# Optimization experiments

Measured on AMD Instinct MI355X. Metric: run time of the kernel, lower is better.

Reference implementation:

```python
import jax, jax.numpy as jnp
import numpy as np

N_NODES = 100000
N_PAIRS = 800000  # undirected pairs; E = 2*N_PAIRS directed edges
D_FEAT = 128
THRESHOLD = 0.01
EPS = 1e-8


def setup_inputs() -> dict:
    key = jax.random.key(0)
    k1, k2, k3, k4 = jax.random.split(key, 4)
    # symmetric edge list without self-loops (each undirected pair in both directions)
    src = jax.random.randint(k1, (N_PAIRS,), 0, N_NODES)
    off = jax.random.randint(k2, (N_PAIRS,), 1, N_NODES)
    dst = (src + off) % N_NODES  # guaranteed != src
    edge_index = jnp.stack([jnp.concatenate([src, dst]),
                            jnp.concatenate([dst, src])]).astype(jnp.int64)
    w_half = jax.random.uniform(k3, (N_PAIRS,), dtype=jnp.float32)
    edge_weight = jnp.concatenate([w_half, w_half])
    features = jax.random.normal(k4, (N_NODES, D_FEAT), dtype=jnp.float32)
    return {"edge_index": edge_index, "edge_weight": edge_weight, "features": features}


def reference(edge_index, edge_weight, features):
    # Cosine-similarity edge dropping (Jaccard.forward, non-binary feature path).
    # Original: build NxN sparse adj, take triu, per-edge cosine sim, zero edges
    # with sim < threshold, symmetrize (triu + triu^T), read back at edge positions.
    # For a symmetric duplicate-free edge list this equals per-edge masking, with
    # diagonal entries doubled by triu + triu^T.
    src, dst = edge_index[0], edge_index[1]
    node_norm = jnp.sqrt(jnp.sum(features * features, axis=-1))  # [N]
    inner = jnp.sum(features[src] * features[dst], axis=-1)       # [E] per-edge gather+dot
    sim = inner / (node_norm[src] * node_norm[dst] + EPS)
    keep = (sim >= THRESHOLD).astype(edge_weight.dtype)
    diag_double = 1.0 + (src == dst).astype(edge_weight.dtype)    # triu+triu^T doubles diagonal
    return edge_weight * keep * diag_double
```

## Files before the change

kernel.cpp:

```cpp
#include <hip/hip_runtime.h>
#include <hip/hip_fp16.h>

#define D_FEAT 128
#define THRESH 0.01f
#define EPS_F  1e-8f


__device__ float edge_out_scalar(const float* __restrict__ feat,
                                 float w, int s, int d) {
#pragma clang fp contract(off)
    const float* fs = feat + (size_t)s * D_FEAT;
    const float* fd = feat + (size_t)d * D_FEAT;
    float r[8], rs[8], rd[8];
#pragma unroll
    for (int j = 0; j < 8; ++j) {
        float a = fs[j], b = fd[j];
        r[j]  = a * b;
        rs[j] = a * a;
        rd[j] = b * b;
    }
    for (int k = 1; k < 16; ++k) {
#pragma unroll
        for (int j = 0; j < 8; ++j) {
            float a = fs[8 * k + j], b = fd[8 * k + j];
            r[j]  = r[j]  + a * b;
            rs[j] = rs[j] + a * a;
            rd[j] = rd[j] + b * b;
        }
    }
    float inner = ((r[0]  + r[1])  + (r[2]  + r[3]))  + ((r[4]  + r[5])  + (r[6]  + r[7]));
    float ss    = ((rs[0] + rs[1]) + (rs[2] + rs[3])) + ((rs[4] + rs[5]) + (rs[6] + rs[7]));
    float dd    = ((rd[0] + rd[1]) + (rd[2] + rd[3])) + ((rd[4] + rd[5]) + (rd[6] + rd[7]));
    float ns = __fsqrt_rn(ss);
    float nd = __fsqrt_rn(dd);
    float denom = ns * nd + EPS_F;
    float sim = inner / denom;
    float keep = (sim >= THRESH) ? 1.0f : 0.0f;
    float diag = (s == d) ? 2.0f : 1.0f;
    return (w * keep) * diag;
}

__device__ __forceinline__ float exact_sim_pairlanes(const float* __restrict__ feat,
                                                     int src, int dst, int h) {
#pragma clang fp contract(off)
    const float4* fs = (const float4*)(feat + (size_t)src * D_FEAT);
    const float4* fd = (const float4*)(feat + (size_t)dst * D_FEAT);
    float r[4], rs[4], rd[4];
    {
        float4 a = fs[h];
        float4 b = fd[h];
        r[0]  = a.x * b.x; r[1]  = a.y * b.y; r[2]  = a.z * b.z; r[3]  = a.w * b.w;
        rs[0] = a.x * a.x; rs[1] = a.y * a.y; rs[2] = a.z * a.z; rs[3] = a.w * a.w;
        rd[0] = b.x * b.x; rd[1] = b.y * b.y; rd[2] = b.z * b.z; rd[3] = b.w * b.w;
    }
#pragma unroll
    for (int k = 1; k < 16; ++k) {
        float4 a = fs[2 * k + h];
        float4 b = fd[2 * k + h];
        r[0]  = r[0]  + a.x * b.x;
        r[1]  = r[1]  + a.y * b.y;
        r[2]  = r[2]  + a.z * b.z;
        r[3]  = r[3]  + a.w * b.w;
        rs[0] = rs[0] + a.x * a.x;
        rs[1] = rs[1] + a.y * a.y;
        rs[2] = rs[2] + a.z * a.z;
        rs[3] = rs[3] + a.w * a.w;
        rd[0] = rd[0] + b.x * b.x;
        rd[1] = rd[1] + b.y * b.y;
        rd[2] = rd[2] + b.z * b.z;
        rd[3] = rd[3] + b.w * b.w;
    }
    float A  = (r[0]  + r[1])  + (r[2]  + r[3]);
    float As = (rs[0] + rs[1]) + (rs[2] + rs[3]);
    float Ad = (rd[0] + rd[1]) + (rd[2] + rd[3]);

    float inner = A  + __shfl_xor(A, 1, 64);
    float ssE   = As + __shfl_xor(As, 1, 64);
    float ddE   = Ad + __shfl_xor(Ad, 1, 64);

    float ns    = __fsqrt_rn(ssE);
    float nd    = __fsqrt_rn(ddE);
    float den   = ns * nd + EPS_F;
    return inner / den;
}

__global__ __launch_bounds__(256) void jaccard_edge_kernel(
    const int* __restrict__ ei, const float* __restrict__ w,
    const float* __restrict__ feat, float* __restrict__ out,
    int P, int E)
{
    int t    = blockIdx.x * blockDim.x + threadIdx.x;
    int pair = t >> 1;
    int half = t & 1;
    if (pair >= P) return;

    int src = ei[pair];
    int dst = ei[E + pair];

    float sim  = exact_sim_pairlanes(feat, src, dst, half);
    float keep = (sim >= THRESH) ? 1.0f : 0.0f;

    if (half == 0) {
        float diag = (src == dst) ? 2.0f : 1.0f;
        out[pair] = (w[pair] * keep) * diag;
        int m = P + pair;
        if (m < E) {
            int s2 = ei[m];
            int d2 = ei[E + m];
            if (s2 == dst && d2 == src) out[m] = (w[m] * keep) * diag;
            else                        out[m] = edge_out_scalar(feat, w[m], s2, d2);
        }
    }
}

__global__ __launch_bounds__(256) void convert_f16_kernel(
    const float* __restrict__ feat, __half* __restrict__ hfeat, int n8)
{
    int t = blockIdx.x * blockDim.x + threadIdx.x;
    if (t >= n8) return;
    const float4* p = (const float4*)feat + 2 * (size_t)t;
    float4 a = p[0];
    float4 b = p[1];
    __half2 h0 = __floats2half2_rn(a.x, a.y);
    __half2 h1 = __floats2half2_rn(a.z, a.w);
    __half2 h2 = __floats2half2_rn(b.x, b.y);
    __half2 h3 = __floats2half2_rn(b.z, b.w);
    uint4 o;
    o.x = *reinterpret_cast<unsigned int*>(&h0);
    o.y = *reinterpret_cast<unsigned int*>(&h1);
    o.z = *reinterpret_cast<unsigned int*>(&h2);
    o.w = *reinterpret_cast<unsigned int*>(&h3);
    reinterpret_cast<uint4*>(hfeat)[(size_t)t] = o;
}

__device__ __forceinline__ void acc2(unsigned int ua, unsigned int ub,
                                     float& dot, float& sab, float& ss, float& dd) {
    float2 fa = __half22float2(*reinterpret_cast<const __half2*>(&ua));
    float2 fb = __half22float2(*reinterpret_cast<const __half2*>(&ub));
    float p0 = fa.x * fb.x, p1 = fa.y * fb.y;
    dot += p0 + p1;
    sab += fabsf(p0) + fabsf(p1);
    ss  += fa.x * fa.x + fa.y * fa.y;
    dd  += fb.x * fb.x + fb.y * fb.y;
}

__global__ __launch_bounds__(256) void jaccard_edge_f16_kernel(
    const int* __restrict__ ei, const float* __restrict__ w,
    const float* __restrict__ feat, const __half* __restrict__ hfeat,
    float* __restrict__ out, int P, int E)
{
    int t    = blockIdx.x * blockDim.x + threadIdx.x;
    int pair = t >> 2;
    int q    = t & 3;
    if (pair >= P) return;

    int src = ei[pair];
    int dst = ei[E + pair];

    const uint4* ha = (const uint4*)(hfeat + (size_t)src * D_FEAT);
    const uint4* hb = (const uint4*)(hfeat + (size_t)dst * D_FEAT);

    float dot = 0.f, sab = 0.f, ss = 0.f, dd = 0.f;
#pragma unroll
    for (int k = 0; k < 4; ++k) {
        uint4 ua = ha[4 * k + q];
        uint4 ub = hb[4 * k + q];
        acc2(ua.x, ub.x, dot, sab, ss, dd);
        acc2(ua.y, ub.y, dot, sab, ss, dd);
        acc2(ua.z, ub.z, dot, sab, ss, dd);
        acc2(ua.w, ub.w, dot, sab, ss, dd);
    }
    dot += __shfl_xor(dot, 1, 64); dot += __shfl_xor(dot, 2, 64);
    sab += __shfl_xor(sab, 1, 64); sab += __shfl_xor(sab, 2, 64);
    ss  += __shfl_xor(ss,  1, 64); ss  += __shfl_xor(ss,  2, 64);
    dd  += __shfl_xor(dd,  1, 64); dd  += __shfl_xor(dd,  2, 64);

    float na  = __fsqrt_rn(ss);
    float nb  = __fsqrt_rn(dd);
    float den = na * nb + EPS_F;
    float sim = dot / den;

    float bnd = 1.2e-3f * (sab / den) + 1.2e-3f * fabsf(sim)
              + 3.5e-7f * (1.0f / na + 1.0f / nb) + 1e-7f;
    float diff = sim - THRESH;

    float keep;
    if (fabsf(diff) > bnd) {
        keep = (diff >= 0.f) ? 1.0f : 0.0f;
    } else {
        float se = 0.f;
        if (q < 2) se = exact_sim_pairlanes(feat, src, dst, q);
        keep = (se >= THRESH) ? 1.0f : 0.0f;
    }

    if (q == 0) {
        float diag = (src == dst) ? 2.0f : 1.0f;
        out[pair] = (w[pair] * keep) * diag;
        int m = P + pair;
        if (m < E) {
            int s2 = ei[m];
            int d2 = ei[E + m];
            if (s2 == dst && d2 == src) out[m] = (w[m] * keep) * diag;
            else                        out[m] = edge_out_scalar(feat, w[m], s2, d2);
        }
    }
}

extern "C" void kernel_launch(void* const* d_in, const int* in_sizes, int n_in,
                              void* d_out, int out_size, void* d_ws, size_t ws_size,
                              hipStream_t stream) {
    const int*   ei   = (const int*)d_in[0];
    const float* w    = (const float*)d_in[1];
    const float* feat = (const float*)d_in[2];
    float*       out  = (float*)d_out;

    int E = in_sizes[1];
    int P = E - E / 2;
    long nfeat = in_sizes[2];
    size_t need = (size_t)nfeat * sizeof(__half);

    if (ws_size < need || (nfeat & 7) != 0) {
        int threads = 2 * P;
        int grid = (threads + 255) / 256;
        jaccard_edge_kernel<<<grid, 256, 0, stream>>>(ei, w, feat, out, P, E);
        return;
    }

    __half* hfeat = (__half*)d_ws;
    int n8 = (int)(nfeat / 8);
    convert_f16_kernel<<<(n8 + 255) / 256, 256, 0, stream>>>(feat, hfeat, n8);

    int threads = 4 * P;
    int grid = (threads + 255) / 256;
    jaccard_edge_f16_kernel<<<grid, 256, 0, stream>>>(ei, w, feat, hfeat, out, P, E);
}
```

Before: 155.9 us.

## Precompute exact per-node norms and use fdot2 f16 dot with two lanes per pair

The conversion kernel now also computes each node's exact fp32 norm, using the same summation order as the original, and stores it in workspace. The edge kernel reads these norms, so it no longer reduces squared norms per edge, and it computes the half-precision dot product with packed fdot2 instructions, two lanes per pair. The fallback for borderline edges now only recomputes the exact inner product. Each lane holds more data in registers, and the error bound is a new heuristic that could misclassify edges if it is too loose.

```diff
diff --git a/kernel.cpp b/kernel.cpp
--- a/kernel.cpp
+++ b/kernel.cpp
@@ -4,6 +4,8 @@
 #define D_FEAT 128
 #define THRESH 0.01f
 #define EPS_F  1e-8f
+
+typedef _Float16 half2_t __attribute__((ext_vector_type(2)));
 
 
 __device__ float edge_out_scalar(const float* __restrict__ feat,
@@ -57,18 +59,12 @@
     for (int k = 1; k < 16; ++k) {
         float4 a = fs[2 * k + h];
         float4 b = fd[2 * k + h];
-        r[0]  = r[0]  + a.x * b.x;
-        r[1]  = r[1]  + a.y * b.y;
-        r[2]  = r[2]  + a.z * b.z;
-        r[3]  = r[3]  + a.w * b.w;
-        rs[0] = rs[0] + a.x * a.x;
-        rs[1] = rs[1] + a.y * a.y;
-        rs[2] = rs[2] + a.z * a.z;
-        rs[3] = rs[3] + a.w * a.w;
-        rd[0] = rd[0] + b.x * b.x;
-        rd[1] = rd[1] + b.y * b.y;
-        rd[2] = rd[2] + b.z * b.z;
-        rd[3] = rd[3] + b.w * b.w;
+        r[0]  = r[0]  + a.x * b.x;  r[1]  = r[1]  + a.y * b.y;
+        r[2]  = r[2]  + a.z * b.z;  r[3]  = r[3]  + a.w * b.w;
+        rs[0] = rs[0] + a.x * a.x;  rs[1] = rs[1] + a.y * a.y;
+        rs[2] = rs[2] + a.z * a.z;  rs[3] = rs[3] + a.w * a.w;
+        rd[0] = rd[0] + b.x * b.x;  rd[1] = rd[1] + b.y * b.y;
+        rd[2] = rd[2] + b.z * b.z;  rd[3] = rd[3] + b.w * b.w;
     }
     float A  = (r[0]  + r[1])  + (r[2]  + r[3]);
     float As = (rs[0] + rs[1]) + (rs[2] + rs[3]);
@@ -82,6 +78,28 @@
     float nd    = __fsqrt_rn(ddE);
     float den   = ns * nd + EPS_F;
     return inner / den;
+}
+
+__device__ __forceinline__ float exact_inner_pairlanes(const float* __restrict__ feat,
+                                                       int src, int dst, int h) {
+#pragma clang fp contract(off)
+    const float4* fs = (const float4*)(feat + (size_t)src * D_FEAT);
+    const float4* fd = (const float4*)(feat + (size_t)dst * D_FEAT);
+    float r[4];
+    {
+        float4 a = fs[h];
+        float4 b = fd[h];
+        r[0] = a.x * b.x; r[1] = a.y * b.y; r[2] = a.z * b.z; r[3] = a.w * b.w;
+    }
+#pragma unroll
+    for (int k = 1; k < 16; ++k) {
+        float4 a = fs[2 * k + h];
+        float4 b = fd[2 * k + h];
+        r[0] = r[0] + a.x * b.x;  r[1] = r[1] + a.y * b.y;
+        r[2] = r[2] + a.z * b.z;  r[3] = r[3] + a.w * b.w;
+    }
+    float A = (r[0] + r[1]) + (r[2] + r[3]);
+    return A + __shfl_xor(A, 1, 64);
 }
 
 __global__ __launch_bounds__(256) void jaccard_edge_kernel(
@@ -113,45 +131,68 @@
     }
 }
 
-__global__ __launch_bounds__(256) void convert_f16_kernel(
-    const float* __restrict__ feat, __half* __restrict__ hfeat, int n8)
+__global__ __launch_bounds__(256) void norm_convert_kernel(
+    const float* __restrict__ feat, __half* __restrict__ hfeat,
+    float* __restrict__ nrm, int nNodes)
 {
+#pragma clang fp contract(off)
     int t = blockIdx.x * blockDim.x + threadIdx.x;
-    if (t >= n8) return;
-    const float4* p = (const float4*)feat + 2 * (size_t)t;
-    float4 a = p[0];
-    float4 b = p[1];
-    __half2 h0 = __floats2half2_rn(a.x, a.y);
-    __half2 h1 = __floats2half2_rn(a.z, a.w);
-    __half2 h2 = __floats2half2_rn(b.x, b.y);
-    __half2 h3 = __floats2half2_rn(b.z, b.w);
-    uint4 o;
-    o.x = *reinterpret_cast<unsigned int*>(&h0);
-    o.y = *reinterpret_cast<unsigned int*>(&h1);
-    o.z = *reinterpret_cast<unsigned int*>(&h2);
-    o.w = *reinterpret_cast<unsigned int*>(&h3);
-    reinterpret_cast<uint4*>(hfeat)[(size_t)t] = o;
-}
-
-__device__ __forceinline__ void acc2(unsigned int ua, unsigned int ub,
-                                     float& dot, float& sab, float& ss, float& dd) {
-    float2 fa = __half22float2(*reinterpret_cast<const __half2*>(&ua));
-    float2 fb = __half22float2(*reinterpret_cast<const __half2*>(&ub));
-    float p0 = fa.x * fb.x, p1 = fa.y * fb.y;
-    dot += p0 + p1;
-    sab += fabsf(p0) + fabsf(p1);
-    ss  += fa.x * fa.x + fa.y * fa.y;
-    dd  += fb.x * fb.x + fb.y * fb.y;
-}
-
-__global__ __launch_bounds__(256) void jaccard_edge_f16_kernel(
+    int node = t >> 1;
+    int h    = t & 1;
+    if (node >= nNodes) return;
+
+    const float4* fs  = (const float4*)(feat + (size_t)node * D_FEAT);
+    uint2*        hro = (uint2*)(hfeat + (size_t)node * D_FEAT);
+
+    float rs[4];
+    {
+        float4 a = fs[h];
+        rs[0] = a.x * a.x; rs[1] = a.y * a.y; rs[2] = a.z * a.z; rs[3] = a.w * a.w;
+        __half2 h0 = __floats2half2_rn(a.x, a.y);
+        __half2 h1 = __floats2half2_rn(a.z, a.w);
+        uint2 o;
+        o.x = __builtin_bit_cast(unsigned int, h0);
+        o.y = __builtin_bit_cast(unsigned int, h1);
+        hro[h] = o;
+    }
+#pragma unroll
+    for (int k = 1; k < 16; ++k) {
+        float4 a = fs[2 * k + h];
+        rs[0] = rs[0] + a.x * a.x;  rs[1] = rs[1] + a.y * a.y;
+        rs[2] = rs[2] + a.z * a.z;  rs[3] = rs[3] + a.w * a.w;
+        __half2 h0 = __floats2half2_rn(a.x, a.y);
+        __half2 h1 = __floats2half2_rn(a.z, a.w);
+        uint2 o;
+        o.x = __builtin_bit_cast(unsigned int, h0);
+        o.y = __builtin_bit_cast(unsigned int, h1);
+        hro[2 * k + h] = o;
+    }
+    float As = (rs[0] + rs[1]) + (rs[2] + rs[3]);
+    float ss = As + __shfl_xor(As, 1, 64);
+    if (h == 0) nrm[node] = __fsqrt_rn(ss);
+}
+
+__device__ __forceinline__ float dot8_f16(uint4 ua, uint4 ub, float acc) {
+    acc = __builtin_amdgcn_fdot2(__builtin_bit_cast(half2_t, ua.x),
+                                 __builtin_bit_cast(half2_t, ub.x), acc, false);
+    acc = __builtin_amdgcn_fdot2(__builtin_bit_cast(half2_t, ua.y),
+                                 __builtin_bit_cast(half2_t, ub.y), acc, false);
+    acc = __builtin_amdgcn_fdot2(__builtin_bit_cast(half2_t, ua.z),
+                                 __builtin_bit_cast(half2_t, ub.z), acc, false);
+    acc = __builtin_amdgcn_fdot2(__builtin_bit_cast(half2_t, ua.w),
+                                 __builtin_bit_cast(half2_t, ub.w), acc, false);
+    return acc;
+}
+
+__global__ __launch_bounds__(256) void jaccard_edge_f16n_kernel(
     const int* __restrict__ ei, const float* __restrict__ w,
     const float* __restrict__ feat, const __half* __restrict__ hfeat,
-    float* __restrict__ out, int P, int E)
+    const float* __restrict__ nrm, float* __restrict__ out, int P, int E)
 {
+#pragma clang fp contract(off)
     int t    = blockIdx.x * blockDim.x + threadIdx.x;
-    int pair = t >> 2;
-    int q    = t & 3;
+    int pair = t >> 1;
+    int h    = t & 1;
     if (pair >= P) return;
 
     int src = ei[pair];
@@ -160,40 +201,38 @@
     const uint4* ha = (const uint4*)(hfeat + (size_t)src * D_FEAT);
     const uint4* hb = (const uint4*)(hfeat + (size_t)dst * D_FEAT);
 
-    float dot = 0.f, sab = 0.f, ss = 0.f, dd = 0.f;
-#pragma unroll
-    for (int k = 0; k < 4; ++k) {
-        uint4 ua = ha[4 * k + q];
-        uint4 ub = hb[4 * k + q];
-        acc2(ua.x, ub.x, dot, sab, ss, dd);
-        acc2(ua.y, ub.y, dot, sab, ss, dd);
-        acc2(ua.z, ub.z, dot, sab, ss, dd);
-        acc2(ua.w, ub.w, dot, sab, ss, dd);
-    }
-    dot += __shfl_xor(dot, 1, 64); dot += __shfl_xor(dot, 2, 64);
-    sab += __shfl_xor(sab, 1, 64); sab += __shfl_xor(sab, 2, 64);
-    ss  += __shfl_xor(ss,  1, 64); ss  += __shfl_xor(ss,  2, 64);
-    dd  += __shfl_xor(dd,  1, 64); dd  += __shfl_xor(dd,  2, 64);
-
-    float na  = __fsqrt_rn(ss);
-    float nb  = __fsqrt_rn(dd);
-    float den = na * nb + EPS_F;
-    float sim = dot / den;
-
-    float bnd = 1.2e-3f * (sab / den) + 1.2e-3f * fabsf(sim)
-              + 3.5e-7f * (1.0f / na + 1.0f / nb) + 1e-7f;
+    uint4 A[8], B[8];
+#pragma unroll
+    for (int k = 0; k < 8; ++k) {
+        A[k] = ha[2 * k + h];
+        B[k] = hb[2 * k + h];
+    }
+    float na = nrm[src];
+    float nb = nrm[dst];
+
+    float d = 0.f;
+#pragma unroll
+    for (int k = 0; k < 8; ++k) d = dot8_f16(A[k], B[k], d);
+
+    float dot = d + __shfl_xor(d, 1, 64);
+
+    float prod = na * nb;
+    float den  = prod + EPS_F;
+    float sim  = dot / den;
+
+    float bnd  = (1.1e-3f * prod + 4e-7f * (na + nb)) / den + 1e-6f;
     float diff = sim - THRESH;
 
     float keep;
     if (fabsf(diff) > bnd) {
         keep = (diff >= 0.f) ? 1.0f : 0.0f;
     } else {
-        float se = 0.f;
-        if (q < 2) se = exact_sim_pairlanes(feat, src, dst, q);
+        float inner = exact_inner_pairlanes(feat, src, dst, h);
+        float se    = inner / den;
         keep = (se >= THRESH) ? 1.0f : 0.0f;
     }
 
-    if (q == 0) {
+    if (h == 0) {
         float diag = (src == dst) ? 2.0f : 1.0f;
         out[pair] = (w[pair] * keep) * diag;
         int m = P + pair;
@@ -217,9 +256,10 @@
     int E = in_sizes[1];
     int P = E - E / 2;
     long nfeat = in_sizes[2];
-    size_t need = (size_t)nfeat * sizeof(__half);
-
-    if (ws_size < need || (nfeat & 7) != 0) {
+    long nNodes = nfeat / D_FEAT;
+    size_t need = (size_t)nfeat * sizeof(__half) + (size_t)nNodes * sizeof(float);
+
+    if (ws_size < need || (nfeat % D_FEAT) != 0) {
         int threads = 2 * P;
         int grid = (threads + 255) / 256;
         jaccard_edge_kernel<<<grid, 256, 0, stream>>>(ei, w, feat, out, P, E);
@@ -227,10 +267,12 @@
     }
 
     __half* hfeat = (__half*)d_ws;
-    int n8 = (int)(nfeat / 8);
-    convert_f16_kernel<<<(n8 + 255) / 256, 256, 0, stream>>>(feat, hfeat, n8);
-
-    int threads = 4 * P;
-    int grid = (threads + 255) / 256;
-    jaccard_edge_f16_kernel<<<grid, 256, 0, stream>>>(ei, w, feat, hfeat, out, P, E);
-}
+    float*  nrm   = (float*)((char*)d_ws + (size_t)nfeat * sizeof(__half));
+
+    int tA = 2 * (int)nNodes;
+    norm_convert_kernel<<<(tA + 255) / 256, 256, 0, stream>>>(feat, hfeat, nrm, (int)nNodes);
+
+    int tB = 2 * P;
+    jaccard_edge_f16n_kernel<<<(tB + 255) / 256, 256, 0, stream>>>(
+        ei, w, feat, hfeat, nrm, out, P, E);
+}
```

Measured after the change: 171.2 us. 1.1x slower.
